# Kernel tuning notes

Measured on AMD Instinct MI355X. Metric: run time of the kernel, lower is better.

## Reference

```python
import jax, jax.numpy as jnp
import numpy as np

B, N, F, DEG = 64, 1024, 128, 8
K1, K2, K3 = 512, 256, 128  # ceil(0.5*N) cascaded pool sizes
NUM_CLASSES = 10
E = B * N * DEG

def _elu(x):
    return jnp.where(x > 0, x, jnp.expm1(x))

def gcn(x, W, b, src, dst, ev, n):
    # PyG GCNConv with improved=True: self-loop weight 2, symmetric norm
    h = x @ W
    w = ev.astype(h.dtype)
    deg = jax.ops.segment_sum(w, dst, num_segments=n) + 2.0
    dinv = jax.lax.rsqrt(deg)
    coef = (w * dinv[src] * dinv[dst])[:, None]
    out = jax.ops.segment_sum(h[src] * coef, dst, num_segments=n)
    out = out + h * (2.0 * dinv * dinv)[:, None]  # self-loop term
    return out + b

def topk_pool(x, p, src, dst, ev, bg, npg, k):
    # score = tanh(x.p/||p||); keep top-k per graph; mask+remap edges
    score = jnp.tanh((x @ p) / jnp.linalg.norm(p))
    vals, idx = jax.lax.top_k(score.reshape(bg, npg), k)
    perm = (idx + (jnp.arange(bg) * npg)[:, None]).reshape(-1)
    x_new = x[perm] * vals.reshape(-1)[:, None]
    remap = jnp.full((bg * npg,), -1, jnp.int32).at[perm].set(
        jnp.arange(bg * k, dtype=jnp.int32))
    s2, d2 = remap[src], remap[dst]
    ev2 = ev & (s2 >= 0) & (d2 >= 0)
    return x_new, jnp.maximum(s2, 0), jnp.maximum(d2, 0), ev2, perm

def setup_inputs() -> dict:
    key = jax.random.key(0)
    ks = jax.random.split(key, 16)
    offs = (jnp.arange(B) * N)[:, None]
    e_per = DEG * N
    src = (jax.random.randint(ks[0], (B, e_per), 0, N) + offs).reshape(-1).astype(jnp.int32)
    dst = (jax.random.randint(ks[1], (B, e_per), 0, N) + offs).reshape(-1).astype(jnp.int32)
    def w(k, shape, fan_in):
        return jax.random.normal(k, shape, jnp.float32) / np.sqrt(fan_in)
    return {
        "x": jax.random.normal(ks[2], (B * N, F), jnp.float32),
        "W1": w(ks[3], (F, 32), F), "b1": jnp.zeros((32,)), "p1": w(ks[4], (32,), 32),
        "W2": w(ks[5], (32, 64), 32), "b2": jnp.zeros((64,)), "p2": w(ks[6], (64,), 64),
        "W3": w(ks[7], (64, 128), 64), "b3": jnp.zeros((128,)), "p3": w(ks[8], (128,), 128),
        "W4": w(ks[9], (128, 256), 128), "b4": jnp.zeros((256,)),
        "W5": w(ks[10], (384, 128), 384), "b5": jnp.zeros((128,)),
        "W6": w(ks[11], (192, 64), 192), "b6": jnp.zeros((64,)),
        "W7": w(ks[12], (96, 32), 96), "b7": jnp.zeros((32,)),
        "Wl": w(ks[13], (64, 64), 64),
        "Wc": w(ks[14], (64, NUM_CLASSES), 64), "bc": jnp.zeros((NUM_CLASSES,)),
        "src": src, "dst": dst,
    }

def reference(x, W1, b1, p1, W2, b2, p2, W3, b3, p3, W4, b4,
              W5, b5, W6, b6, W7, b7, Wl, Wc, bc, src, dst):
    ev0 = jnp.ones((E,), bool)
    x1 = _elu(gcn(x, W1, b1, src, dst, ev0, B * N))
    x2, s2, d2, ev2, idx2 = topk_pool(x1, p1, src, dst, ev0, B, N, K1)
    x2 = _elu(x2)
    x3 = _elu(gcn(x2, W2, b2, s2, d2, ev2, B * K1))
    x4, s4, d4, ev4, idx4 = topk_pool(x3, p2, s2, d2, ev2, B, K1, K2)
    x4 = _elu(x4)
    x5 = _elu(gcn(x4, W3, b3, s4, d4, ev4, B * K2))
    x6, s6, d6, ev6, idx6 = topk_pool(x5, p3, s4, d4, ev4, B, K2, K3)
    x6 = _elu(x6)
    x7 = _elu(gcn(x6, W4, b4, s6, d6, ev6, B * K3))
    x8 = jnp.zeros((B * K2, 256), x7.dtype).at[idx6].set(x7)
    x8 = _elu(jnp.concatenate([x8, x5], axis=1))
    x9 = _elu(gcn(x8, W5, b5, s4, d4, ev4, B * K2))
    x10 = jnp.zeros((B * K1, 128), x9.dtype).at[idx4].set(x9)
    x10 = _elu(jnp.concatenate([x10, x3], axis=1))
    x11 = _elu(gcn(x10, W6, b6, s2, d2, ev2, B * K1))
    x12 = jnp.zeros((B * N, 64), x11.dtype).at[idx2].set(x11)
    x12 = _elu(jnp.concatenate([x12, x1], axis=1))
    x13 = _elu(gcn(x12, W7, b7, src, dst, ev0, B * N))
    batch = jnp.repeat(jnp.arange(B), N)
    gmp = jax.ops.segment_max(x13, batch, num_segments=B)
    gap = jax.ops.segment_sum(x13, batch, num_segments=B) / N
    g = _elu(jnp.concatenate([gmp, gap], axis=1))
    g = _elu(g @ Wl)
    logits = g @ Wc + bc
    return jax.nn.log_softmax(logits, axis=-1)
```

## Files before the change

kernel.cpp:

```cpp
#include <hip/hip_runtime.h>
#include <hip/hip_bf16.h>
#include <math.h>

#define B_ 64
#define N_ 1024
#define E_ 524288
#define EPG_ 8192
#define K1_ 512
#define K2_ 256
#define K3_ 128
#define M0_ 65536
#define M1_ 32768
#define M2_ 16384
#define M3_ 8192

static __device__ __forceinline__ float eluf(float x){ return x > 0.f ? x : expm1f(x); }
static __device__ __forceinline__ unsigned short f2bf(float f){
  union{float f; unsigned u;} v; v.f=f;
  unsigned u = v.u + 0x7FFF + ((v.u>>16)&1);
  return (unsigned short)(u>>16);
}
static __device__ __forceinline__ float bf2f(unsigned short h){
  union{unsigned u; float f;} v; v.u = ((unsigned)h)<<16;
  return v.f;
}
static __device__ __forceinline__ float4 ldU4(const unsigned short* __restrict__ p, size_t idx){
  ushort4 r = *(const ushort4*)(p + idx);
  float4 o; o.x=bf2f(r.x); o.y=bf2f(r.y); o.z=bf2f(r.z); o.w=bf2f(r.w);
  return o;
}
static __device__ __forceinline__ void stU4(unsigned short* __restrict__ p, size_t idx, float4 v){
  ushort4 h; h.x=f2bf(v.x); h.y=f2bf(v.y); h.z=f2bf(v.z); h.w=f2bf(v.w);
  *(ushort4*)(p + idx) = h;
}

template<int BM,int BN,int MODE>
__global__ __launch_bounds__(256) void k_mm(const float* __restrict__ Xf,
    const unsigned short* __restrict__ Xh,
    const float* __restrict__ W, unsigned short* __restrict__ H, int M, int K, int N,
    const int* __restrict__ perm, const float* __restrict__ vals,
    const unsigned short* __restrict__ Xd, const int* __restrict__ orig,
    const int* __restrict__ rm, int WD4){
  constexpr int TX = BN/4;
  constexpr int TY = 256/TX;
  constexpr int RM = BM/TY;
  __shared__ float Xs[BM][36];
  __shared__ float Ws[32][BN];
  const int t = threadIdx.x;
  const int tx = t % TX, ty = t / TX;
  const int m0 = blockIdx.x*BM, n0 = blockIdx.y*BN;
  float acc[RM][4];
  #pragma unroll
  for (int r=0;r<RM;++r){acc[r][0]=0.f;acc[r][1]=0.f;acc[r][2]=0.f;acc[r][3]=0.f;}
  for (int k0=0;k0<K;k0+=32){
    #pragma unroll
    for (int l=0;l<BM/32;++l){
      int fi=l*256+t, row=fi>>3, q=fi&7;
      int m = m0+row;
      int c4 = (k0>>2)+q;
      float4 v;
      if (MODE==0){
        v = *(const float4*)(Xf + (size_t)m*K + (c4<<2));
      } else if (MODE==1){
        int pm = perm[m]; float vv = vals[m];
        float4 h = ldU4(Xh, (size_t)pm*K + (c4<<2));
        v.x=eluf(h.x*vv); v.y=eluf(h.y*vv); v.z=eluf(h.z*vv); v.w=eluf(h.w*vv);
      } else {
        if (c4 < WD4){
          int o = orig ? orig[m] : m;
          int j = rm[o];
          if (j>=0){
            float4 h = ldU4(Xd, ((size_t)j*WD4 + c4)*4);
            v.x=eluf(h.x); v.y=eluf(h.y); v.z=eluf(h.z); v.w=eluf(h.w);
          } else { v.x=0.f;v.y=0.f;v.z=0.f;v.w=0.f; }
        } else {
          int ws4 = (K>>2) - WD4;
          float4 h = ldU4(Xh, ((size_t)m*ws4 + (c4-WD4))*4);
          v.x=eluf(h.x); v.y=eluf(h.y); v.z=eluf(h.z); v.w=eluf(h.w);
        }
      }
      *(float4*)(&Xs[row][q*4]) = v;
    }
    #pragma unroll
    for (int l=0;l<BN/32;++l){
      int fi=l*256+t, wrow=fi/(BN/4), wq=fi%(BN/4);
      *(float4*)(&Ws[wrow][wq*4]) = *(const float4*)(W + (size_t)(k0+wrow)*N + n0 + wq*4);
    }
    __syncthreads();
    #pragma unroll
    for (int kq=0;kq<32;kq+=4){
      float4 xv[RM];
      #pragma unroll
      for (int r=0;r<RM;++r) xv[r] = *(const float4*)(&Xs[ty*RM+r][kq]);
      #pragma unroll
      for (int j=0;j<4;++j){
        float4 wv = *(const float4*)(&Ws[kq+j][tx*4]);
        #pragma unroll
        for (int r=0;r<RM;++r){
          float xs = (j==0)?xv[r].x:(j==1)?xv[r].y:(j==2)?xv[r].z:xv[r].w;
          acc[r][0]=fmaf(xs,wv.x,acc[r][0]);
          acc[r][1]=fmaf(xs,wv.y,acc[r][1]);
          acc[r][2]=fmaf(xs,wv.z,acc[r][2]);
          acc[r][3]=fmaf(xs,wv.w,acc[r][3]);
        }
      }
    }
    __syncthreads();
  }
  #pragma unroll
  for (int r=0;r<RM;++r){
    int m = m0 + ty*RM + r;
    float4 h; h.x=acc[r][0];h.y=acc[r][1];h.z=acc[r][2];h.w=acc[r][3];
    stU4(H, (size_t)m*N + n0 + tx*4, h);
  }
}

__global__ __launch_bounds__(1024) void k_csr(const int* __restrict__ src0,
    const int* __restrict__ dst0, int* __restrict__ rowptr,
    int* __restrict__ col, float* __restrict__ dinv){
  __shared__ int ldeg[1024];
  __shared__ int ps[1024];
  __shared__ int lcur[1024];
  const int g = blockIdx.x, t = threadIdx.x;
  const int ebase = g*EPG_, nbase = g<<10;
  ldeg[t] = 0;
  __syncthreads();
  #pragma unroll
  for (int i=0;i<EPG_/1024;++i){
    int e = ebase + i*1024 + t;
    atomicAdd(&ldeg[dst0[e] - nbase], 1);
  }
  __syncthreads();
  int d = ldeg[t];
  ps[t] = d; __syncthreads();
  for (int o=1;o<1024;o<<=1){
    int v = (t>=o) ? ps[t-o] : 0;
    __syncthreads(); ps[t] += v; __syncthreads();
  }
  int excl = ps[t] - d;
  rowptr[nbase + t] = ebase + excl;
  lcur[t] = excl;
  dinv[nbase + t] = rsqrtf((float)d + 2.f);
  if (g == B_-1 && t == 1023) rowptr[M0_] = E_;
  __syncthreads();
  #pragma unroll
  for (int i=0;i<EPG_/1024;++i){
    int e = ebase + i*1024 + t;
    int dl = dst0[e] - nbase;
    int p = atomicAdd(&lcur[dl], 1);
    col[ebase + p] = src0[e];
  }
}

__global__ __launch_bounds__(1024) void k_pool(const float* __restrict__ score,
    int npg, int K, const int* __restrict__ prevOrig,
    const int* __restrict__ rowptr0, const int* __restrict__ col0,
    int* __restrict__ perm, float* __restrict__ vals,
    int* __restrict__ orig, int* __restrict__ rm, float* __restrict__ dinv){
  __shared__ float ss[1024]; __shared__ int si[1024];
  const int g = blockIdx.x, t = threadIdx.x;
  for (int i=t; i<1024; i+=npg) rm[(g<<10)+i] = -1;
  ss[t] = score[g*npg + t]; si[t] = t;
  __syncthreads();
  for (int k=2;k<=npg;k<<=1){
    for (int j=k>>1;j>0;j>>=1){
      int ixj = t ^ j;
      if (ixj > t){
        float s1=ss[t], s2=ss[ixj]; int i1=si[t], i2=si[ixj];
        bool aAfterB = (s1 < s2) || (s1==s2 && i1 > i2);
        bool sw = ((t & k)==0) ? aAfterB : !aAfterB;
        if (sw){ ss[t]=s2; si[t]=i2; ss[ixj]=s1; si[ixj]=i1; }
      }
      __syncthreads();
    }
  }
  int o = -1;
  if (t < K){
    int pl = g*npg + si[t];
    perm[g*K+t] = pl;
    vals[g*K+t] = ss[t];
    o = prevOrig ? prevOrig[pl] : pl;
    orig[g*K+t] = o;
    rm[o] = g*K + t;
  }
  __syncthreads();
  if (t < K){
    int beg = rowptr0[o], end = rowptr0[o+1];
    int d = 0;
    for (int j=beg;j<end;++j) d += (rm[col0[j]] >= 0) ? 1 : 0;
    dinv[g*K+t] = rsqrtf((float)d + 2.f);
  }
}

template<int F, bool SCORE>
__global__ __launch_bounds__(256) void k_gather(const int* __restrict__ rowptr,
    const int* __restrict__ col, const float* __restrict__ dinv,
    const unsigned short* __restrict__ H, const float* __restrict__ bias,
    unsigned short* __restrict__ OUT, int M,
    const float* __restrict__ p, float* __restrict__ score){
  constexpr int FQ = F/4;
  int i = blockIdx.x*256+threadIdx.x;
  if (i >= M*FQ) return;
  int n = i/FQ, q = i - (i/FQ)*FQ;
  int beg = rowptr[n], end = rowptr[n+1];
  float4 acc; acc.x=0.f;acc.y=0.f;acc.z=0.f;acc.w=0.f;
  for (int j=beg;j<end;++j){
    int s = col[j];
    float c = dinv[s];
    float4 h = ldU4(H, (size_t)s*F + q*4);
    acc.x=fmaf(c,h.x,acc.x); acc.y=fmaf(c,h.y,acc.y);
    acc.z=fmaf(c,h.z,acc.z); acc.w=fmaf(c,h.w,acc.w);
  }
  float dn = dinv[n];
  float sc = 2.f*dn*dn;
  float4 hn = ldU4(H, (size_t)n*F + q*4);
  float4 bv = *(const float4*)(bias + q*4);
  float4 o;
  o.x = eluf(fmaf(sc,hn.x,fmaf(dn,acc.x,bv.x)));
  o.y = eluf(fmaf(sc,hn.y,fmaf(dn,acc.y,bv.y)));
  o.z = eluf(fmaf(sc,hn.z,fmaf(dn,acc.z,bv.z)));
  o.w = eluf(fmaf(sc,hn.w,fmaf(dn,acc.w,bv.w)));
  stU4(OUT, (size_t)n*F + q*4, o);
  if (SCORE){
    float4 pv = *(const float4*)(p + q*4);
    float dot = o.x*pv.x + o.y*pv.y + o.z*pv.z + o.w*pv.w;
    float n2  = pv.x*pv.x + pv.y*pv.y + pv.z*pv.z + pv.w*pv.w;
    #pragma unroll
    for (int mk=FQ>>1; mk>0; mk>>=1){
      dot += __shfl_xor(dot, mk);
      n2  += __shfl_xor(n2,  mk);
    }
    if (q==0) score[n] = tanhf(dot * rsqrtf(n2));
  }
}

template<int F, bool SCORE>
__global__ __launch_bounds__(256) void k_gather_rm(const int* __restrict__ orig,
    const int* __restrict__ rowptr0, const int* __restrict__ col0,
    const int* __restrict__ rm, const float* __restrict__ dinv,
    const unsigned short* __restrict__ H, const float* __restrict__ bias,
    unsigned short* __restrict__ OUT, int M,
    const float* __restrict__ p, float* __restrict__ score){
  constexpr int FQ = F/4;
  int i = blockIdx.x*256+threadIdx.x;
  if (i >= M*FQ) return;
  int n = i/FQ, q = i - (i/FQ)*FQ;
  int o = orig[n];
  int beg = rowptr0[o], end = rowptr0[o+1];
  float4 acc; acc.x=0.f;acc.y=0.f;acc.z=0.f;acc.w=0.f;
  for (int j=beg;j<end;++j){
    int s = rm[col0[j]];
    if (s >= 0){
      float c = dinv[s];
      float4 h = ldU4(H, (size_t)s*F + q*4);
      acc.x=fmaf(c,h.x,acc.x); acc.y=fmaf(c,h.y,acc.y);
      acc.z=fmaf(c,h.z,acc.z); acc.w=fmaf(c,h.w,acc.w);
    }
  }
  float dn = dinv[n];
  float sc = 2.f*dn*dn;
  float4 hn = ldU4(H, (size_t)n*F + q*4);
  float4 bv = *(const float4*)(bias + q*4);
  float4 ov;
  ov.x = eluf(fmaf(sc,hn.x,fmaf(dn,acc.x,bv.x)));
  ov.y = eluf(fmaf(sc,hn.y,fmaf(dn,acc.y,bv.y)));
  ov.z = eluf(fmaf(sc,hn.z,fmaf(dn,acc.z,bv.z)));
  ov.w = eluf(fmaf(sc,hn.w,fmaf(dn,acc.w,bv.w)));
  stU4(OUT, (size_t)n*F + q*4, ov);
  if (SCORE){
    float4 pv = *(const float4*)(p + q*4);
    float dot = ov.x*pv.x + ov.y*pv.y + ov.z*pv.z + ov.w*pv.w;
    float n2  = pv.x*pv.x + pv.y*pv.y + pv.z*pv.z + pv.w*pv.w;
    #pragma unroll
    for (int mk=FQ>>1; mk>0; mk>>=1){
      dot += __shfl_xor(dot, mk);
      n2  += __shfl_xor(n2,  mk);
    }
    if (q==0) score[n] = tanhf(dot * rsqrtf(n2));
  }
}

__global__ void k_head(const unsigned short* __restrict__ x13, const float* __restrict__ Wl,
                       const float* __restrict__ Wc, const float* __restrict__ bc,
                       float* __restrict__ out){
  __shared__ float smax[256], ssum[256];
  __shared__ float gv[64], g2[64], logit[10];
  int g = blockIdx.x, t = threadIdx.x;
  int f = t & 31, r0 = t >> 5;
  float mx = -3.4e38f, sm = 0.f;
  const unsigned short* base = x13 + (size_t)g*N_*32;
  for (int r=r0; r<N_; r+=8){ float v = bf2f(base[r*32+f]); mx = fmaxf(mx,v); sm += v; }
  smax[t]=mx; ssum[t]=sm; __syncthreads();
  if (t<128){ smax[t]=fmaxf(smax[t],smax[t+128]); ssum[t]+=ssum[t+128]; } __syncthreads();
  if (t<64){ smax[t]=fmaxf(smax[t],smax[t+64]); ssum[t]+=ssum[t+64]; } __syncthreads();
  if (t<32){
    float m2 = fmaxf(smax[t],smax[t+32]); float s2 = ssum[t]+ssum[t+32];
    gv[t] = eluf(m2); gv[32+t] = eluf(s2 * (1.f/N_));
  }
  __syncthreads();
  if (t<64){
    float acc=0.f;
    #pragma unroll
    for (int i2=0;i2<64;++i2) acc = fmaf(gv[i2], Wl[i2*64+t], acc);
    g2[t] = eluf(acc);
  }
  __syncthreads();
  if (t<10){
    float acc = bc[t];
    #pragma unroll
    for (int j=0;j<64;++j) acc = fmaf(g2[j], Wc[j*10+t], acc);
    logit[t] = acc;
  }
  __syncthreads();
  if (t==0){
    float m=-3.4e38f; for (int c=0;c<10;++c) m=fmaxf(m,logit[c]);
    float s=0.f; for (int c=0;c<10;++c) s += expf(logit[c]-m);
    float lse = m + logf(s);
    for (int c=0;c<10;++c) out[g*10+c] = logit[c]-lse;
  }
}

extern "C" void kernel_launch(void* const* d_in, const int* in_sizes, int n_in,
                              void* d_out, int out_size, void* d_ws, size_t ws_size,
                              hipStream_t stream){
  const float* x  = (const float*)d_in[0];
  const float* W1 = (const float*)d_in[1];
  const float* b1 = (const float*)d_in[2];
  const float* p1 = (const float*)d_in[3];
  const float* W2 = (const float*)d_in[4];
  const float* b2 = (const float*)d_in[5];
  const float* p2 = (const float*)d_in[6];
  const float* W3 = (const float*)d_in[7];
  const float* b3 = (const float*)d_in[8];
  const float* p3 = (const float*)d_in[9];
  const float* W4 = (const float*)d_in[10];
  const float* b4 = (const float*)d_in[11];
  const float* W5 = (const float*)d_in[12];
  const float* b5 = (const float*)d_in[13];
  const float* W6 = (const float*)d_in[14];
  const float* b6 = (const float*)d_in[15];
  const float* W7 = (const float*)d_in[16];
  const float* b7 = (const float*)d_in[17];
  const float* Wl = (const float*)d_in[18];
  const float* Wc = (const float*)d_in[19];
  const float* bc = (const float*)d_in[20];
  const int* src0 = (const int*)d_in[21];
  const int* dst0 = (const int*)d_in[22];
  float* out = (float*)d_out;

  char* wsp = (char*)d_ws;
  size_t off = 0;
  auto alloc = [&](size_t bytes)->char*{
    char* p = wsp + off;
    off += (bytes + 255) & ~(size_t)255;
    return p;
  };
  unsigned short* bufA = (unsigned short*)alloc((size_t)2097152*2);
  unsigned short* bufB = (unsigned short*)alloc((size_t)2097152*2);
  unsigned short* bufC = (unsigned short*)alloc((size_t)2097152*2);
  unsigned short* bufD = (unsigned short*)alloc((size_t)2097152*2);
  unsigned short* bufH = (unsigned short*)alloc((size_t)2097152*2);
  float* score= (float*)alloc((size_t)M0_*4);
  float* vals2= (float*)alloc((size_t)M1_*4);
  float* vals4= (float*)alloc((size_t)M2_*4);
  float* vals6= (float*)alloc((size_t)M3_*4);
  int* idx2 = (int*)alloc((size_t)M1_*4);
  int* idx4 = (int*)alloc((size_t)M2_*4);
  int* idx6 = (int*)alloc((size_t)M3_*4);
  int* orig4 = (int*)alloc((size_t)M2_*4);
  int* orig6 = (int*)alloc((size_t)M3_*4);
  int* rm02 = (int*)alloc((size_t)M0_*4);
  int* rm04 = (int*)alloc((size_t)M0_*4);
  int* rm06 = (int*)alloc((size_t)M0_*4);
  int* col0 = (int*)alloc((size_t)E_*4);
  int* rowptr0 = (int*)alloc((size_t)(M0_+1)*4);
  float* dinv0 = (float*)alloc((size_t)M0_*4);
  float* dinv2 = (float*)alloc((size_t)M1_*4);
  float* dinv4 = (float*)alloc((size_t)M2_*4);
  float* dinv6 = (float*)alloc((size_t)M3_*4);

  auto NB = [](int total){ return (total+255)/256; };

  k_csr<<<B_,1024,0,stream>>>(src0, dst0, rowptr0, col0, dinv0);

  k_mm<128,32,0><<<dim3(M0_/128,1),256,0,stream>>>(x, nullptr, W1, bufH, M0_, 128, 32,
      nullptr,nullptr,nullptr,nullptr,nullptr,0);
  k_gather<32,true><<<NB(M0_*8),256,0,stream>>>(rowptr0, col0, dinv0, bufH, b1, bufA, M0_, p1, score);

  k_pool<<<B_,1024,0,stream>>>(score, 1024, K1_, nullptr, rowptr0, col0,
      idx2, vals2, idx2, rm02, dinv2);

  k_mm<64,64,1><<<dim3(M1_/64,1),256,0,stream>>>(nullptr, bufA, W2, bufH, M1_, 32, 64,
      idx2, vals2, nullptr,nullptr,nullptr,0);
  k_gather_rm<64,true><<<NB(M1_*16),256,0,stream>>>(idx2, rowptr0, col0, rm02, dinv2, bufH, b2, bufB, M1_, p2, score);

  k_pool<<<B_,512,0,stream>>>(score, 512, K2_, idx2, rowptr0, col0,
      idx4, vals4, orig4, rm04, dinv4);

  k_mm<64,64,1><<<dim3(M2_/64,2),256,0,stream>>>(nullptr, bufB, W3, bufH, M2_, 64, 128,
      idx4, vals4, nullptr,nullptr,nullptr,0);
  k_gather_rm<128,true><<<NB(M2_*32),256,0,stream>>>(orig4, rowptr0, col0, rm04, dinv4, bufH, b3, bufC, M2_, p3, score);

  k_pool<<<B_,256,0,stream>>>(score, 256, K3_, orig4, rowptr0, col0,
      idx6, vals6, orig6, rm06, dinv6);

  k_mm<64,64,1><<<dim3(M3_/64,4),256,0,stream>>>(nullptr, bufC, W4, bufH, M3_, 128, 256,
      idx6, vals6, nullptr,nullptr,nullptr,0);
  k_gather_rm<256,false><<<NB(M3_*64),256,0,stream>>>(orig6, rowptr0, col0, rm06, dinv6, bufH, b4, bufD, M3_, nullptr, nullptr);

  k_mm<64,64,2><<<dim3(M2_/64,2),256,0,stream>>>(nullptr, bufC, W5, bufH, M2_, 384, 128,
      nullptr,nullptr, bufD, orig4, rm06, 64);
  k_gather_rm<128,false><<<NB(M2_*32),256,0,stream>>>(orig4, rowptr0, col0, rm04, dinv4, bufH, b5, bufD, M2_, nullptr, nullptr);

  k_mm<64,64,2><<<dim3(M1_/64,1),256,0,stream>>>(nullptr, bufB, W6, bufH, M1_, 192, 64,
      nullptr,nullptr, bufD, idx2, rm04, 32);
  k_gather_rm<64,false><<<NB(M1_*16),256,0,stream>>>(idx2, rowptr0, col0, rm02, dinv2, bufH, b6, bufC, M1_, nullptr, nullptr);

  k_mm<128,32,2><<<dim3(M0_/128,1),256,0,stream>>>(nullptr, bufA, W7, bufH, M0_, 96, 32,
      nullptr,nullptr, bufC, nullptr, rm02, 16);
  k_gather<32,false><<<NB(M0_*8),256,0,stream>>>(rowptr0, col0, dinv0, bufH, b7, bufA, M0_, nullptr, nullptr);

  k_head<<<B_,256,0,stream>>>(bufA, Wl, Wc, bc, out);

  (void)in_sizes; (void)n_in; (void)out_size; (void)ws_size;
}
```

Measured before the change: 327.9 us.

## Fuse CSR build with first matmul and top-k pooling into gather kernels

Merges the CSR construction and the first feature matmul into one launch by giving them disjoint block ranges, so the two independent jobs run concurrently. Each top-k pooling step is folded into the preceding gather kernel: blocks atomically count completions per graph, and the last block for a graph (after a thread fence) does the bitonic sort and remap with 256 threads. This removes four kernel launches and their serialization gaps. In exchange, pooling now runs on 256-thread blocks looping over up to 1024 elements, and correctness relies on the per-graph completion counters and fences.

```diff
diff --git a/kernel.cpp b/kernel.cpp
--- a/kernel.cpp
+++ b/kernel.cpp
@@ -35,8 +35,7 @@
 }
 
 template<int BM,int BN,int MODE>
-__global__ __launch_bounds__(256) void k_mm(const float* __restrict__ Xf,
-    const unsigned short* __restrict__ Xh,
+__global__ __launch_bounds__(256) void k_mm(const unsigned short* __restrict__ Xh,
     const float* __restrict__ W, unsigned short* __restrict__ H, int M, int K, int N,
     const int* __restrict__ perm, const float* __restrict__ vals,
     const unsigned short* __restrict__ Xd, const int* __restrict__ orig,
@@ -59,9 +58,7 @@
       int m = m0+row;
       int c4 = (k0>>2)+q;
       float4 v;
-      if (MODE==0){
-        v = *(const float4*)(Xf + (size_t)m*K + (c4<<2));
-      } else if (MODE==1){
+      if (MODE==1){
         int pm = perm[m]; float vv = vals[m];
         float4 h = ldU4(Xh, (size_t)pm*K + (c4<<2));
         v.x=eluf(h.x*vv); v.y=eluf(h.y*vv); v.z=eluf(h.z*vv); v.w=eluf(h.w*vv);
@@ -115,168 +112,273 @@
   }
 }
 
-__global__ __launch_bounds__(1024) void k_csr(const int* __restrict__ src0,
-    const int* __restrict__ dst0, int* __restrict__ rowptr,
-    int* __restrict__ col, float* __restrict__ dinv){
-  __shared__ int ldeg[1024];
-  __shared__ int ps[1024];
-  __shared__ int lcur[1024];
-  const int g = blockIdx.x, t = threadIdx.x;
-  const int ebase = g*EPG_, nbase = g<<10;
-  ldeg[t] = 0;
-  __syncthreads();
-  #pragma unroll
-  for (int i=0;i<EPG_/1024;++i){
-    int e = ebase + i*1024 + t;
-    atomicAdd(&ldeg[dst0[e] - nbase], 1);
-  }
-  __syncthreads();
-  int d = ldeg[t];
-  ps[t] = d; __syncthreads();
-  for (int o=1;o<1024;o<<=1){
-    int v = (t>=o) ? ps[t-o] : 0;
-    __syncthreads(); ps[t] += v; __syncthreads();
-  }
-  int excl = ps[t] - d;
-  rowptr[nbase + t] = ebase + excl;
-  lcur[t] = excl;
-  dinv[nbase + t] = rsqrtf((float)d + 2.f);
-  if (g == B_-1 && t == 1023) rowptr[M0_] = E_;
-  __syncthreads();
-  #pragma unroll
-  for (int i=0;i<EPG_/1024;++i){
-    int e = ebase + i*1024 + t;
-    int dl = dst0[e] - nbase;
-    int p = atomicAdd(&lcur[dl], 1);
-    col[ebase + p] = src0[e];
-  }
-}
-
-__global__ __launch_bounds__(1024) void k_pool(const float* __restrict__ score,
-    int npg, int K, const int* __restrict__ prevOrig,
-    const int* __restrict__ rowptr0, const int* __restrict__ col0,
-    int* __restrict__ perm, float* __restrict__ vals,
-    int* __restrict__ orig, int* __restrict__ rm, float* __restrict__ dinv){
-  __shared__ float ss[1024]; __shared__ int si[1024];
-  const int g = blockIdx.x, t = threadIdx.x;
-  for (int i=t; i<1024; i+=npg) rm[(g<<10)+i] = -1;
-  ss[t] = score[g*npg + t]; si[t] = t;
+__global__ __launch_bounds__(256) void k_csr_mm1(const float* __restrict__ X,
+    const float* __restrict__ W, unsigned short* __restrict__ H,
+    const int* __restrict__ src0, const int* __restrict__ dst0,
+    int* __restrict__ rowptr, int* __restrict__ col, float* __restrict__ dinv,
+    int* __restrict__ cntA, int* __restrict__ cntB, int* __restrict__ cntC){
+  const int t = threadIdx.x;
+  if (blockIdx.x < 512){
+    constexpr int BM=128, BN=32, TX=BN/4, TY=256/TX, RM=BM/TY;
+    constexpr int K=128, N=32;
+    __shared__ float Xs[BM][36];
+    __shared__ float Ws[32][BN];
+    const int tx = t % TX, ty = t / TX;
+    const int m0 = blockIdx.x*BM;
+    float acc[RM][4];
+    #pragma unroll
+    for (int r=0;r<RM;++r){acc[r][0]=0.f;acc[r][1]=0.f;acc[r][2]=0.f;acc[r][3]=0.f;}
+    for (int k0=0;k0<K;k0+=32){
+      #pragma unroll
+      for (int l=0;l<BM/32;++l){
+        int fi=l*256+t, row=fi>>3, q=fi&7;
+        *(float4*)(&Xs[row][q*4]) =
+            *(const float4*)(X + (size_t)(m0+row)*K + k0 + q*4);
+      }
+      {
+        int wrow=t/(BN/4), wq=t%(BN/4);
+        *(float4*)(&Ws[wrow][wq*4]) = *(const float4*)(W + (size_t)(k0+wrow)*N + wq*4);
+      }
+      __syncthreads();
+      #pragma unroll
+      for (int kq=0;kq<32;kq+=4){
+        float4 xv[RM];
+        #pragma unroll
+        for (int r=0;r<RM;++r) xv[r] = *(const float4*)(&Xs[ty*RM+r][kq]);
+        #pragma unroll
+        for (int j=0;j<4;++j){
+          float4 wv = *(const float4*)(&Ws[kq+j][tx*4]);
+          #pragma unroll
+          for (int r=0;r<RM;++r){
+            float xs = (j==0)?xv[r].x:(j==1)?xv[r].y:(j==2)?xv[r].z:xv[r].w;
+            acc[r][0]=fmaf(xs,wv.x,acc[r][0]);
+            acc[r][1]=fmaf(xs,wv.y,acc[r][1]);
+            acc[r][2]=fmaf(xs,wv.z,acc[r][2]);
+            acc[r][3]=fmaf(xs,wv.w,acc[r][3]);
+          }
+        }
+      }
+      __syncthreads();
+    }
+    #pragma unroll
+    for (int r=0;r<RM;++r){
+      int m = m0 + ty*RM + r;
+      float4 h; h.x=acc[r][0];h.y=acc[r][1];h.z=acc[r][2];h.w=acc[r][3];
+      stU4(H, (size_t)m*N + tx*4, h);
+    }
+  } else {
+    __shared__ int ldeg[1024];
+    __shared__ int pspart[256];
+    __shared__ int lcur[1024];
+    const int g = blockIdx.x - 512;
+    const int ebase = g*EPG_, nbase = g<<10;
+    for (int v=t; v<1024; v+=256) ldeg[v]=0;
+    __syncthreads();
+    #pragma unroll
+    for (int i=0;i<EPG_/256;++i){
+      int e = ebase + i*256 + t;
+      atomicAdd(&ldeg[dst0[e]-nbase], 1);
+    }
+    __syncthreads();
+    int s4[4]; int sum=0;
+    #pragma unroll
+    for (int i=0;i<4;++i){ s4[i]=ldeg[t*4+i]; sum+=s4[i]; }
+    pspart[t]=sum; __syncthreads();
+    for (int o=1;o<256;o<<=1){
+      int v2 = (t>=o)?pspart[t-o]:0;
+      __syncthreads(); pspart[t]+=v2; __syncthreads();
+    }
+    int run = pspart[t]-sum;
+    #pragma unroll
+    for (int i=0;i<4;++i){
+      int node = t*4+i;
+      rowptr[nbase+node] = ebase + run;
+      lcur[node] = run;
+      dinv[nbase+node] = rsqrtf((float)s4[i] + 2.f);
+      run += s4[i];
+    }
+    if (g == B_-1 && t == 255) rowptr[M0_] = E_;
+    __syncthreads();
+    #pragma unroll
+    for (int i=0;i<EPG_/256;++i){
+      int e = ebase + i*256 + t;
+      int dl = dst0[e]-nbase;
+      int p = atomicAdd(&lcur[dl], 1);
+      col[ebase+p] = src0[e];
+    }
+    if (t==0){ cntA[g]=0; cntB[g]=0; cntC[g]=0; }
+  }
+}
+
+static __device__ void pool_phase(int g, int npg, const float* __restrict__ score,
+    const int* __restrict__ prevOrig, const int* __restrict__ rowptr0,
+    const int* __restrict__ col0, int* __restrict__ perm, float* __restrict__ vals,
+    int* __restrict__ orig, int* __restrict__ rm, float* __restrict__ dinv,
+    float* ss, int* si){
+  const int t = threadIdx.x;
+  for (int v=t; v<npg; v+=256){ ss[v]=score[g*npg+v]; si[v]=v; }
+  for (int v=t; v<1024; v+=256) rm[(g<<10)+v] = -1;
   __syncthreads();
   for (int k=2;k<=npg;k<<=1){
     for (int j=k>>1;j>0;j>>=1){
-      int ixj = t ^ j;
-      if (ixj > t){
-        float s1=ss[t], s2=ss[ixj]; int i1=si[t], i2=si[ixj];
-        bool aAfterB = (s1 < s2) || (s1==s2 && i1 > i2);
-        bool sw = ((t & k)==0) ? aAfterB : !aAfterB;
-        if (sw){ ss[t]=s2; si[t]=i2; ss[ixj]=s1; si[ixj]=i1; }
+      for (int v=t; v<npg; v+=256){
+        if ((v & j)==0){
+          int ix = v|j;
+          float s1=ss[v], s2=ss[ix]; int i1=si[v], i2=si[ix];
+          bool aAfterB = (s1 < s2) || (s1==s2 && i1 > i2);
+          bool sw = ((v & k)==0) ? aAfterB : !aAfterB;
+          if (sw){ ss[v]=s2; si[v]=i2; ss[ix]=s1; si[ix]=i1; }
+        }
       }
       __syncthreads();
     }
   }
-  int o = -1;
-  if (t < K){
-    int pl = g*npg + si[t];
-    perm[g*K+t] = pl;
-    vals[g*K+t] = ss[t];
-    o = prevOrig ? prevOrig[pl] : pl;
-    orig[g*K+t] = o;
-    rm[o] = g*K + t;
+  const int KK = npg>>1;
+  for (int v=t; v<KK; v+=256){
+    int pl = g*npg + si[v];
+    perm[g*KK+v] = pl;
+    vals[g*KK+v] = ss[v];
+    int o = prevOrig ? prevOrig[pl] : pl;
+    orig[g*KK+v] = o;
+    rm[o] = g*KK + v;
   }
   __syncthreads();
-  if (t < K){
+  for (int v=t; v<KK; v+=256){
+    int o = orig[g*KK+v];
     int beg = rowptr0[o], end = rowptr0[o+1];
     int d = 0;
     for (int j=beg;j<end;++j) d += (rm[col0[j]] >= 0) ? 1 : 0;
-    dinv[g*K+t] = rsqrtf((float)d + 2.f);
-  }
-}
-
-template<int F, bool SCORE>
+    dinv[g*KK+v] = rsqrtf((float)d + 2.f);
+  }
+}
+
+template<int F, bool SCORE, bool POOL>
 __global__ __launch_bounds__(256) void k_gather(const int* __restrict__ rowptr,
     const int* __restrict__ col, const float* __restrict__ dinv,
     const unsigned short* __restrict__ H, const float* __restrict__ bias,
     unsigned short* __restrict__ OUT, int M,
-    const float* __restrict__ p, float* __restrict__ score){
+    const float* __restrict__ p, float* __restrict__ score,
+    int npg, const int* __restrict__ prevOrig,
+    int* __restrict__ permOut, float* __restrict__ valsOut,
+    int* __restrict__ origOut, int* __restrict__ rmOut,
+    float* __restrict__ dinvOut, int* __restrict__ cnt){
   constexpr int FQ = F/4;
   int i = blockIdx.x*256+threadIdx.x;
-  if (i >= M*FQ) return;
-  int n = i/FQ, q = i - (i/FQ)*FQ;
-  int beg = rowptr[n], end = rowptr[n+1];
-  float4 acc; acc.x=0.f;acc.y=0.f;acc.z=0.f;acc.w=0.f;
-  for (int j=beg;j<end;++j){
-    int s = col[j];
-    float c = dinv[s];
-    float4 h = ldU4(H, (size_t)s*F + q*4);
-    acc.x=fmaf(c,h.x,acc.x); acc.y=fmaf(c,h.y,acc.y);
-    acc.z=fmaf(c,h.z,acc.z); acc.w=fmaf(c,h.w,acc.w);
-  }
-  float dn = dinv[n];
-  float sc = 2.f*dn*dn;
-  float4 hn = ldU4(H, (size_t)n*F + q*4);
-  float4 bv = *(const float4*)(bias + q*4);
-  float4 o;
-  o.x = eluf(fmaf(sc,hn.x,fmaf(dn,acc.x,bv.x)));
-  o.y = eluf(fmaf(sc,hn.y,fmaf(dn,acc.y,bv.y)));
-  o.z = eluf(fmaf(sc,hn.z,fmaf(dn,acc.z,bv.z)));
-  o.w = eluf(fmaf(sc,hn.w,fmaf(dn,acc.w,bv.w)));
-  stU4(OUT, (size_t)n*F + q*4, o);
-  if (SCORE){
-    float4 pv = *(const float4*)(p + q*4);
-    float dot = o.x*pv.x + o.y*pv.y + o.z*pv.z + o.w*pv.w;
-    float n2  = pv.x*pv.x + pv.y*pv.y + pv.z*pv.z + pv.w*pv.w;
-    #pragma unroll
-    for (int mk=FQ>>1; mk>0; mk>>=1){
-      dot += __shfl_xor(dot, mk);
-      n2  += __shfl_xor(n2,  mk);
-    }
-    if (q==0) score[n] = tanhf(dot * rsqrtf(n2));
-  }
-}
-
-template<int F, bool SCORE>
+  if (i < M*FQ){
+    int n = i/FQ, q = i - (i/FQ)*FQ;
+    int beg = rowptr[n], end = rowptr[n+1];
+    float4 acc; acc.x=0.f;acc.y=0.f;acc.z=0.f;acc.w=0.f;
+    for (int j=beg;j<end;++j){
+      int s = col[j];
+      float c = dinv[s];
+      float4 h = ldU4(H, (size_t)s*F + q*4);
+      acc.x=fmaf(c,h.x,acc.x); acc.y=fmaf(c,h.y,acc.y);
+      acc.z=fmaf(c,h.z,acc.z); acc.w=fmaf(c,h.w,acc.w);
+    }
+    float dn = dinv[n];
+    float sc = 2.f*dn*dn;
+    float4 hn = ldU4(H, (size_t)n*F + q*4);
+    float4 bv = *(const float4*)(bias + q*4);
+    float4 o;
+    o.x = eluf(fmaf(sc,hn.x,fmaf(dn,acc.x,bv.x)));
+    o.y = eluf(fmaf(sc,hn.y,fmaf(dn,acc.y,bv.y)));
+    o.z = eluf(fmaf(sc,hn.z,fmaf(dn,acc.z,bv.z)));
+    o.w = eluf(fmaf(sc,hn.w,fmaf(dn,acc.w,bv.w)));
+    stU4(OUT, (size_t)n*F + q*4, o);
+    if (SCORE){
+      float4 pv = *(const float4*)(p + q*4);
+      float dot = o.x*pv.x + o.y*pv.y + o.z*pv.z + o.w*pv.w;
+      float n2  = pv.x*pv.x + pv.y*pv.y + pv.z*pv.z + pv.w*pv.w;
+      #pragma unroll
+      for (int mk=FQ>>1; mk>0; mk>>=1){
+        dot += __shfl_xor(dot, mk);
+        n2  += __shfl_xor(n2,  mk);
+      }
+      if (q==0) score[n] = tanhf(dot * rsqrtf(n2));
+    }
+  }
+  if (POOL){
+    __shared__ float ss[1024];
+    __shared__ int si[1024];
+    __shared__ int isLast;
+    __threadfence();
+    int g = blockIdx.x >> 5;
+    if (threadIdx.x==0){
+      int old = atomicAdd(&cnt[g], 1);
+      isLast = (old == 31) ? 1 : 0;
+    }
+    __syncthreads();
+    if (!isLast) return;
+    __threadfence();
+    pool_phase(g, npg, score, prevOrig, rowptr, col, permOut, valsOut,
+               origOut, rmOut, dinvOut, ss, si);
+  }
+}
+
+template<int F, bool SCORE, bool POOL>
 __global__ __launch_bounds__(256) void k_gather_rm(const int* __restrict__ orig,
     const int* __restrict__ rowptr0, const int* __restrict__ col0,
     const int* __restrict__ rm, const float* __restrict__ dinv,
     const unsigned short* __restrict__ H, const float* __restrict__ bias,
     unsigned short* __restrict__ OUT, int M,
-    const float* __restrict__ p, float* __restrict__ score){
+    const float* __restrict__ p, float* __restrict__ score,
+    int npg, const int* __restrict__ prevOrig,
+    int* __restrict__ permOut, float* __restrict__ valsOut,
+    int* __restrict__ origOut, int* __restrict__ rmOut,
+    float* __restrict__ dinvOut, int* __restrict__ cnt){
   constexpr int FQ = F/4;
   int i = blockIdx.x*256+threadIdx.x;
-  if (i >= M*FQ) return;
-  int n = i/FQ, q = i - (i/FQ)*FQ;
-  int o = orig[n];
-  int beg = rowptr0[o], end = rowptr0[o+1];
-  float4 acc; acc.x=0.f;acc.y=0.f;acc.z=0.f;acc.w=0.f;
-  for (int j=beg;j<end;++j){
-    int s = rm[col0[j]];
-    if (s >= 0){
-      float c = dinv[s];
-      float4 h = ldU4(H, (size_t)s*F + q*4);
-      acc.x=fmaf(c,h.x,acc.x); acc.y=fmaf(c,h.y,acc.y);
-      acc.z=fmaf(c,h.z,acc.z); acc.w=fmaf(c,h.w,acc.w);
-    }
-  }
-  float dn = dinv[n];
-  float sc = 2.f*dn*dn;
-  float4 hn = ldU4(H, (size_t)n*F + q*4);
-  float4 bv = *(const float4*)(bias + q*4);
-  float4 ov;
-  ov.x = eluf(fmaf(sc,hn.x,fmaf(dn,acc.x,bv.x)));
-  ov.y = eluf(fmaf(sc,hn.y,fmaf(dn,acc.y,bv.y)));
-  ov.z = eluf(fmaf(sc,hn.z,fmaf(dn,acc.z,bv.z)));
-  ov.w = eluf(fmaf(sc,hn.w,fmaf(dn,acc.w,bv.w)));
-  stU4(OUT, (size_t)n*F + q*4, ov);
-  if (SCORE){
-    float4 pv = *(const float4*)(p + q*4);
-    float dot = ov.x*pv.x + ov.y*pv.y + ov.z*pv.z + ov.w*pv.w;
-    float n2  = pv.x*pv.x + pv.y*pv.y + pv.z*pv.z + pv.w*pv.w;
-    #pragma unroll
-    for (int mk=FQ>>1; mk>0; mk>>=1){
-      dot += __shfl_xor(dot, mk);
-      n2  += __shfl_xor(n2,  mk);
-    }
-    if (q==0) score[n] = tanhf(dot * rsqrtf(n2));
+  if (i < M*FQ){
+    int n = i/FQ, q = i - (i/FQ)*FQ;
+    int o = orig[n];
+    int beg = rowptr0[o], end = rowptr0[o+1];
+    float4 acc; acc.x=0.f;acc.y=0.f;acc.z=0.f;acc.w=0.f;
+    for (int j=beg;j<end;++j){
+      int s = rm[col0[j]];
+      if (s >= 0){
+        float c = dinv[s];
+        float4 h = ldU4(H, (size_t)s*F + q*4);
+        acc.x=fmaf(c,h.x,acc.x); acc.y=fmaf(c,h.y,acc.y);
+        acc.z=fmaf(c,h.z,acc.z); acc.w=fmaf(c,h.w,acc.w);
+      }
+    }
+    float dn = dinv[n];
+    float sc = 2.f*dn*dn;
+    float4 hn = ldU4(H, (size_t)n*F + q*4);
+    float4 bv = *(const float4*)(bias + q*4);
+    float4 ov;
+    ov.x = eluf(fmaf(sc,hn.x,fmaf(dn,acc.x,bv.x)));
+    ov.y = eluf(fmaf(sc,hn.y,fmaf(dn,acc.y,bv.y)));
+    ov.z = eluf(fmaf(sc,hn.z,fmaf(dn,acc.z,bv.z)));
+    ov.w = eluf(fmaf(sc,hn.w,fmaf(dn,acc.w,bv.w)));
+    stU4(OUT, (size_t)n*F + q*4, ov);
+    if (SCORE){
+      float4 pv = *(const float4*)(p + q*4);
+      float dot = ov.x*pv.x + ov.y*pv.y + ov.z*pv.z + ov.w*pv.w;
+      float n2  = pv.x*pv.x + pv.y*pv.y + pv.z*pv.z + pv.w*pv.w;
+      #pragma unroll
+      for (int mk=FQ>>1; mk>0; mk>>=1){
+        dot += __shfl_xor(dot, mk);
+        n2  += __shfl_xor(n2,  mk);
+      }
+      if (q==0) score[n] = tanhf(dot * rsqrtf(n2));
+    }
+  }
+  if (POOL){
+    __shared__ float ss[1024];
+    __shared__ int si[1024];
+    __shared__ int isLast;
+    __threadfence();
+    int g = blockIdx.x >> 5;
+    if (threadIdx.x==0){
+      int old = atomicAdd(&cnt[g], 1);
+      isLast = (old == 31) ? 1 : 0;
+    }
+    __syncthreads();
+    if (!isLast) return;
+    __threadfence();
+    pool_phase(g, npg, score, prevOrig, rowptr0, col0, permOut, valsOut,
+               origOut, rmOut, dinvOut, ss, si);
   }
 }
 
@@ -378,47 +480,53 @@
   float* dinv2 = (float*)alloc((size_t)M1_*4);
   float* dinv4 = (float*)alloc((size_t)M2_*4);
   float* dinv6 = (float*)alloc((size_t)M3_*4);
+  int* cntA = (int*)alloc((size_t)B_*4);
+  int* cntB = (int*)alloc((size_t)B_*4);
+  int* cntC = (int*)alloc((size_t)B_*4);
 
   auto NB = [](int total){ return (total+255)/256; };
 
-  k_csr<<<B_,1024,0,stream>>>(src0, dst0, rowptr0, col0, dinv0);
-
-  k_mm<128,32,0><<<dim3(M0_/128,1),256,0,stream>>>(x, nullptr, W1, bufH, M0_, 128, 32,
-      nullptr,nullptr,nullptr,nullptr,nullptr,0);
-  k_gather<32,true><<<NB(M0_*8),256,0,stream>>>(rowptr0, col0, dinv0, bufH, b1, bufA, M0_, p1, score);
-
-  k_pool<<<B_,1024,0,stream>>>(score, 1024, K1_, nullptr, rowptr0, col0,
-      idx2, vals2, idx2, rm02, dinv2);
-
-  k_mm<64,64,1><<<dim3(M1_/64,1),256,0,stream>>>(nullptr, bufA, W2, bufH, M1_, 32, 64,
+  k_csr_mm1<<<576,256,0,stream>>>(x, W1, bufH, src0, dst0, rowptr0, col0, dinv0,
+                                  cntA, cntB, cntC);
+
+  k_gather<32,true,true><<<NB(M0_*8),256,0,stream>>>(rowptr0, col0, dinv0, bufH, b1,
+      bufA, M0_, p1, score, 1024, nullptr, idx2, vals2, idx2, rm02, dinv2, cntA);
+
+  k_mm<64,64,1><<<dim3(M1_/64,1),256,0,stream>>>(bufA, W2, bufH, M1_, 32, 64,
       idx2, vals2, nullptr,nullptr,nullptr,0);
-  k_gather_rm<64,true><<<NB(M1_*16),256,0,stream>>>(idx2, rowptr0, col0, rm02, dinv2, bufH, b2, bufB, M1_, p2, score);
-
-  k_pool<<<B_,512,0,stream>>>(score, 512, K2_, idx2, rowptr0, col0,
-      idx4, vals4, orig4, rm04, dinv4);
-
-  k_mm<64,64,1><<<dim3(M2_/64,2),256,0,stream>>>(nullptr, bufB, W3, bufH, M2_, 64, 128,
+  k_gather_rm<64,true,true><<<NB(M1_*16),256,0,stream>>>(idx2, rowptr0, col0, rm02,
+      dinv2, bufH, b2, bufB, M1_, p2, score, 512, idx2, idx4, vals4, orig4, rm04,
+      dinv4, cntB);
+
+  k_mm<64,64,1><<<dim3(M2_/64,2),256,0,stream>>>(bufB, W3, bufH, M2_, 64, 128,
       idx4, vals4, nullptr,nullptr,nullptr,0);
-  k_gather_rm<128,true><<<NB(M2_*32),256,0,stream>>>(orig4, rowptr0, col0, rm04, dinv4, bufH, b3, bufC, M2_, p3, score);
-
-  k_pool<<<B_,256,0,stream>>>(score, 256, K3_, orig4, rowptr0, col0,
-      idx6, vals6, orig6, rm06, dinv6);
-
-  k_mm<64,64,1><<<dim3(M3_/64,4),256,0,stream>>>(nullptr, bufC, W4, bufH, M3_, 128, 256,
+  k_gather_rm<128,true,true><<<NB(M2_*32),256,0,stream>>>(orig4, rowptr0, col0, rm04,
+      dinv4, bufH, b3, bufC, M2_, p3, score, 256, orig4, idx6, vals6, orig6, rm06,
+      dinv6, cntC);
+
+  k_mm<64,64,1><<<dim3(M3_/64,4),256,0,stream>>>(bufC, W4, bufH, M3_, 128, 256,
       idx6, vals6, nullptr,nullptr,nullptr,0);
-  k_gather_rm<256,false><<<NB(M3_*64),256,0,stream>>>(orig6, rowptr0, col0, rm06, dinv6, bufH, b4, bufD, M3_, nullptr, nullptr);
-
-  k_mm<64,64,2><<<dim3(M2_/64,2),256,0,stream>>>(nullptr, bufC, W5, bufH, M2_, 384, 128,
+  k_gather_rm<256,false,false><<<NB(M3_*64),256,0,stream>>>(orig6, rowptr0, col0, rm06,
+      dinv6, bufH, b4, bufD, M3_, nullptr, nullptr, 0, nullptr, nullptr, nullptr,
+      nullptr, nullptr, nullptr, nullptr);
+
+  k_mm<64,64,2><<<dim3(M2_/64,2),256,0,stream>>>(bufC, W5, bufH, M2_, 384, 128,
       nullptr,nullptr, bufD, orig4, rm06, 64);
-  k_gather_rm<128,false><<<NB(M2_*32),256,0,stream>>>(orig4, rowptr0, col0, rm04, dinv4, bufH, b5, bufD, M2_, nullptr, nullptr);
-
-  k_mm<64,64,2><<<dim3(M1_/64,1),256,0,stream>>>(nullptr, bufB, W6, bufH, M1_, 192, 64,
+  k_gather_rm<128,false,false><<<NB(M2_*32),256,0,stream>>>(orig4, rowptr0, col0, rm04,
+      dinv4, bufH, b5, bufD, M2_, nullptr, nullptr, 0, nullptr, nullptr, nullptr,
+      nullptr, nullptr, nullptr, nullptr);
+
+  k_mm<64,64,2><<<dim3(M1_/64,1),256,0,stream>>>(bufB, W6, bufH, M1_, 192, 64,
       nullptr,nullptr, bufD, idx2, rm04, 32);
-  k_gather_rm<64,false><<<NB(M1_*16),256,0,stream>>>(idx2, rowptr0, col0, rm02, dinv2, bufH, b6, bufC, M1_, nullptr, nullptr);
-
-  k_mm<128,32,2><<<dim3(M0_/128,1),256,0,stream>>>(nullptr, bufA, W7, bufH, M0_, 96, 32,
+  k_gather_rm<64,false,false><<<NB(M1_*16),256,0,stream>>>(idx2, rowptr0, col0, rm02,
+      dinv2, bufH, b6, bufC, M1_, nullptr, nullptr, 0, nullptr, nullptr, nullptr,
+      nullptr, nullptr, nullptr, nullptr);
+
+  k_mm<128,32,2><<<dim3(M0_/128,1),256,0,stream>>>(bufA, W7, bufH, M0_, 96, 32,
       nullptr,nullptr, bufC, nullptr, rm02, 16);
-  k_gather<32,false><<<NB(M0_*8),256,0,stream>>>(rowptr0, col0, dinv0, bufH, b7, bufA, M0_, nullptr, nullptr);
+  k_gather<32,false,false><<<NB(M0_*8),256,0,stream>>>(rowptr0, col0, dinv0, bufH, b7,
+      bufA, M0_, nullptr, nullptr, 0, nullptr, nullptr, nullptr, nullptr, nullptr,
+      nullptr, nullptr);
 
   k_head<<<B_,256,0,stream>>>(bufA, Wl, Wc, bc, out);
 
```

Result: slower. 846.1 us (+158.1%).
